# Kernel tuning notes

Hardware: AMD Instinct MI355X
Metric: run time of the kernel (lower is better)

The kernel has to match this reference:

```python
import jax, jax.numpy as jnp
import numpy as np

# ---- problem dims ----
B, S, C, H, W = 4, 8, 3, 256, 256
P = 68          # keypoints (self.points)
DS = 4          # detector downsample
WIN = 8
STEPS = 10      # Gauss-Newton iterations per frame pair
EPS = 1e-6
GRAY_W = jnp.array([0.299, 0.587, 0.114], dtype=jnp.float32)

# window offsets [K,2] in (x,y)
_rng = jnp.arange(-WIN, WIN + 1, dtype=jnp.float32)
_OFF = jnp.stack(jnp.meshgrid(_rng, _rng, indexing='xy'), -1).reshape(-1, 2)


def setup_inputs() -> dict:
    key = jax.random.key(0)
    k1, k2 = jax.random.split(key)
    inputs = jax.random.normal(k1, (B, S, C, H, W), dtype=jnp.float32)
    Wdet = jax.random.normal(k2, (P, C, 3, 3), dtype=jnp.float32) * 0.1
    bdet = jnp.zeros((P,), dtype=jnp.float32)
    return {"inputs": inputs, "Wdet": Wdet, "bdet": bdet}


def _bilinear(img, xy):
    # img [H,W]; xy [...,2] in (x,y) pixel coords -> sampled values [...]
    x = jnp.clip(xy[..., 0], 0.0, W - 1.001)
    y = jnp.clip(xy[..., 1], 0.0, H - 1.001)
    x0 = jnp.floor(x); y0 = jnp.floor(y)
    wx = x - x0; wy = y - y0
    x0i = x0.astype(jnp.int32); y0i = y0.astype(jnp.int32)
    x1i = jnp.minimum(x0i + 1, W - 1); y1i = jnp.minimum(y0i + 1, H - 1)
    v00 = img[y0i, x0i]; v01 = img[y0i, x1i]
    v10 = img[y1i, x0i]; v11 = img[y1i, x1i]
    return (1 - wy) * ((1 - wx) * v00 + wx * v01) + wy * ((1 - wx) * v10 + wx * v11)


def _grad_xy(img):
    # central differences with edge replication
    px = jnp.pad(img, ((0, 0), (1, 1)), mode='edge')
    py = jnp.pad(img, ((1, 1), (0, 0)), mode='edge')
    gx = (px[:, 2:] - px[:, :-2]) * 0.5
    gy = (py[2:, :] - py[:-2, :]) * 0.5
    return gx, gy


def _lk_track(old, new, pts):
    # one Lucas-Kanade tracking step: old/new [H,W] gray, pts [P,2] -> [P,2]
    gx, gy = _grad_xy(old)
    pos0 = pts[:, None, :] + _OFF[None]            # [P,K,2]
    I0 = _bilinear(old, pos0)                      # [P,K] template patch
    Ix = _bilinear(gx, pos0)
    Iy = _bilinear(gy, pos0)
    Gxx = (Ix * Ix).sum(-1); Gxy = (Ix * Iy).sum(-1); Gyy = (Iy * Iy).sum(-1)
    det = Gxx * Gyy - Gxy * Gxy + EPS
    Ginv = jnp.stack([jnp.stack([Gyy, -Gxy], -1),
                      jnp.stack([-Gxy, Gxx], -1)], -2) / det[:, None, None]  # [P,2,2]

    def step(i, v):
        I1 = _bilinear(new, pos0 + v[:, None, :])  # [P,K]
        err = I0 - I1
        b = jnp.stack([(err * Ix).sum(-1), (err * Iy).sum(-1)], -1)  # [P,2]
        return v + jnp.einsum('pij,pj->pi', Ginv, b)

    v = jax.lax.fori_loop(0, STEPS, step, jnp.zeros_like(pts))
    return pts + v


def _lk_forward_backward(gray, locs):
    # gray [S,H,W], locs [S,P,2] -> nextPts, fbackPts, backPts each [S,P,2]
    def f(pts, frames):
        o, n = frames
        q = _lk_track(o, n, pts)
        return q, q

    # forward: track detector locs of frame 0 through the sequence
    _, fout = jax.lax.scan(f, locs[0], (gray[:-1], gray[1:]))
    nextPts = jnp.concatenate([locs[:1], fout], 0)
    ro, rn = gray[1:][::-1], gray[:-1][::-1]
    # forward-backward: track the forward end point back to frame 0
    _, fbout = jax.lax.scan(f, nextPts[-1], (ro, rn))
    fbackPts = jnp.concatenate([nextPts[-1:], fbout], 0)[::-1]
    # backward: track detector locs of last frame back through the sequence
    _, bout = jax.lax.scan(f, locs[-1], (ro, rn))
    backPts = jnp.concatenate([locs[-1:], bout], 0)[::-1]
    return nextPts, fbackPts, backPts


def _detector(x, Wdet, bdet):
    # x [N,C,H,W] -> heatmaps [N,P,H/DS,W/DS], locs [N,P,2] (pixel coords), scores [N,P]
    hm = jax.lax.conv_general_dilated(
        x, Wdet, window_strides=(DS, DS), padding='SAME',
        dimension_numbers=('NCHW', 'OIHW', 'NCHW')) + bdet[None, :, None, None]
    N, _, Hd, Wd = hm.shape
    flat = hm.reshape(N, P, Hd * Wd)
    prob = jax.nn.softmax(flat, axis=-1)
    ys, xs = jnp.meshgrid(jnp.arange(Hd, dtype=hm.dtype),
                          jnp.arange(Wd, dtype=hm.dtype), indexing='ij')
    ex = (prob * xs.reshape(-1)).sum(-1) * DS   # soft-argmax, upscaled to input px
    ey = (prob * ys.reshape(-1)).sum(-1) * DS
    locs = jnp.stack([ex, ey], -1)
    scos = flat.max(-1)
    return hm, locs, scos


def reference(inputs, Wdet, bdet):
    x = inputs.reshape(B * S, C, H, W)
    hm, locs, scos = _detector(x, Wdet, bdet)
    heatmaps = hm.reshape(B, S, P, H // DS, W // DS)
    batch_locs = locs.reshape(B, S, P, 2)
    batch_scos = scos.reshape(B, S, P)
    gray = jnp.einsum('bschw,c->bshw', inputs, GRAY_W)  # [B,S,H,W]
    nextPts, fbackPts, backPts = jax.vmap(_lk_forward_backward)(gray, batch_locs)
    return heatmaps, batch_locs, batch_scos, nextPts, fbackPts, backPts
```

## Files before the change

kernel.cpp:

```cpp
#include <hip/hip_runtime.h>
#include <math.h>

namespace {
constexpr int Bn = 4, Sn = 8, Cn = 3, Himg = 256, Wimg = 256;
constexpr int Pn = 68, DS = 4, WIN = 8, STEPS = 10;
constexpr int HWi = Himg * Wimg;
constexpr int NIMG = Bn * Sn;
constexpr int HD = Himg / DS, WD = Wimg / DS;
constexpr int Kwin = (2 * WIN + 1) * (2 * WIN + 1);
constexpr int NWAVE = 5;
constexpr int TPB = NWAVE * 64;
}

__global__ __launch_bounds__(256) void gray_kernel(const float* __restrict__ in,
                                                   float* __restrict__ gray) {
    int idx = blockIdx.x * blockDim.x + threadIdx.x;
    int total = NIMG * HWi / 4;
    if (idx >= total) return;
    int img = idx / (HWi / 4);
    int off = idx % (HWi / 4);
    const float* base = in + (size_t)img * 3 * HWi;
    float4 c0 = ((const float4*)(base))[off];
    float4 c1 = ((const float4*)(base + HWi))[off];
    float4 c2 = ((const float4*)(base + 2 * HWi))[off];
    float4 g;
    g.x = 0.299f * c0.x + 0.587f * c1.x + 0.114f * c2.x;
    g.y = 0.299f * c0.y + 0.587f * c1.y + 0.114f * c2.y;
    g.z = 0.299f * c0.z + 0.587f * c1.z + 0.114f * c2.z;
    g.w = 0.299f * c0.w + 0.587f * c1.w + 0.114f * c2.w;
    ((float4*)(gray + (size_t)img * HWi))[off] = g;
}

__global__ __launch_bounds__(256) void conv_kernel(const float* __restrict__ x,
                                                   const float* __restrict__ Wdet,
                                                   const float* __restrict__ bdet,
                                                   float* __restrict__ hm) {
    __shared__ float wsh[Pn * 27];
    __shared__ float bsh[Pn];
    __shared__ float insh[3][3][Wimg];
    int n = blockIdx.x >> 6;
    int oy = blockIdx.x & 63;
    int tid = threadIdx.x;
    for (int t = tid; t < Pn * 27; t += 256) wsh[t] = Wdet[t];
    if (tid < Pn) bsh[tid] = bdet[tid];
    for (int t = tid; t < 3 * 3 * Wimg; t += 256) {
        int c = t / (3 * Wimg);
        int r = (t / Wimg) % 3;
        int col = t % Wimg;
        insh[c][r][col] = x[(size_t)n * 3 * HWi + (size_t)c * HWi + (oy * 4 + r) * Wimg + col];
    }
    __syncthreads();
    int ox = tid & 63;
    int wid = tid >> 6;
    float in_reg[27];
    #pragma unroll
    for (int c = 0; c < 3; c++)
        #pragma unroll
        for (int ky = 0; ky < 3; ky++)
            #pragma unroll
            for (int kx = 0; kx < 3; kx++)
                in_reg[c * 9 + ky * 3 + kx] = insh[c][ky][ox * 4 + kx];
    #pragma unroll
    for (int i = 0; i < 17; i++) {
        int p = wid + i * 4;
        const float* w = &wsh[p * 27];
        float acc = bsh[p];
        #pragma unroll
        for (int j = 0; j < 27; j++) acc += w[j] * in_reg[j];
        hm[(size_t)n * Pn * 4096 + (size_t)p * 4096 + oy * 64 + ox] = acc;
    }
}

__global__ __launch_bounds__(256) void smax_kernel(const float* __restrict__ hm,
                                                   float* __restrict__ locs,
                                                   float* __restrict__ scos) {
    int row = blockIdx.x;
    const float4* r = (const float4*)(hm + (size_t)row * 4096);
    int tid = threadIdx.x;
    float v[16];
    #pragma unroll
    for (int j = 0; j < 4; j++) {
        float4 q = r[tid + 256 * j];
        v[4 * j + 0] = q.x; v[4 * j + 1] = q.y; v[4 * j + 2] = q.z; v[4 * j + 3] = q.w;
    }
    float m = v[0];
    #pragma unroll
    for (int i = 1; i < 16; i++) m = fmaxf(m, v[i]);
    __shared__ float redm[4];
    #pragma unroll
    for (int o = 32; o; o >>= 1) m = fmaxf(m, __shfl_xor(m, o, 64));
    int wid = tid >> 6, lane = tid & 63;
    if (lane == 0) redm[wid] = m;
    __syncthreads();
    m = fmaxf(fmaxf(redm[0], redm[1]), fmaxf(redm[2], redm[3]));
    float s = 0.f, sx = 0.f, sy = 0.f;
    #pragma unroll
    for (int j = 0; j < 4; j++) {
        #pragma unroll
        for (int q = 0; q < 4; q++) {
            int e = (tid + 256 * j) * 4 + q;
            float ev = expf(v[4 * j + q] - m);
            s += ev;
            sx += ev * (float)(e & 63);
            sy += ev * (float)(e >> 6);
        }
    }
    #pragma unroll
    for (int o = 32; o; o >>= 1) {
        s  += __shfl_xor(s, o, 64);
        sx += __shfl_xor(sx, o, 64);
        sy += __shfl_xor(sy, o, 64);
    }
    __shared__ float reds[3][4];
    if (lane == 0) { reds[0][wid] = s; reds[1][wid] = sx; reds[2][wid] = sy; }
    __syncthreads();
    if (tid == 0) {
        float S_ = reds[0][0] + reds[0][1] + reds[0][2] + reds[0][3];
        float SX = reds[1][0] + reds[1][1] + reds[1][2] + reds[1][3];
        float SY = reds[2][0] + reds[2][1] + reds[2][2] + reds[2][3];
        locs[(size_t)row * 2 + 0] = SX / S_ * 4.0f;
        locs[(size_t)row * 2 + 1] = SY / S_ * 4.0f;
        scos[row] = m;
    }
}

template <int CTRL>
__device__ inline float dpp_add(float v) {
    int t = __builtin_amdgcn_update_dpp(0, __builtin_bit_cast(int, v), CTRL, 0xF, 0xF, true);
    return v + __builtin_bit_cast(float, t);
}

__device__ inline float wredw(float v) {
    v = dpp_add<0x111>(v);
    v = dpp_add<0x112>(v);
    v = dpp_add<0x114>(v);
    v = dpp_add<0x118>(v);
    v = dpp_add<0x142>(v);
    v = dpp_add<0x143>(v);
    int s = __builtin_amdgcn_readlane(__builtin_bit_cast(int, v), 63);
    return __builtin_bit_cast(float, s);
}

template <bool FLY>
__device__ inline float px_at(const float* __restrict__ im, int y, int x) {
    int i = y * Wimg + x;
    if constexpr (FLY)
        return 0.299f * im[i] + 0.587f * im[i + HWi] + 0.114f * im[i + 2 * HWi];
    else
        return im[i];
}

template <bool FLY>
__device__ inline float bilin(const float* __restrict__ im, float x, float y) {
    const float XM = (float)(Wimg - 1.001);
    const float YM = (float)(Himg - 1.001);
    x = fminf(fmaxf(x, 0.0f), XM);
    y = fminf(fmaxf(y, 0.0f), YM);
    float x0f = floorf(x), y0f = floorf(y);
    float wx = x - x0f, wy = y - y0f;
    int x0 = (int)x0f, y0 = (int)y0f;
    int x1 = min(x0 + 1, Wimg - 1), y1 = min(y0 + 1, Himg - 1);
    float v00 = px_at<FLY>(im, y0, x0);
    float v01 = px_at<FLY>(im, y0, x1);
    float v10 = px_at<FLY>(im, y1, x0);
    float v11 = px_at<FLY>(im, y1, x1);
    return (1.0f - wy) * ((1.0f - wx) * v00 + wx * v01) + wy * ((1.0f - wx) * v10 + wx * v11);
}

template <bool FLY>
__device__ inline void sample_tpl(const float* __restrict__ im, float x, float y,
                                  float& I0, float& Ix, float& Iy) {
    const float XM = (float)(Wimg - 1.001);
    const float YM = (float)(Himg - 1.001);
    x = fminf(fmaxf(x, 0.0f), XM);
    y = fminf(fmaxf(y, 0.0f), YM);
    float x0f = floorf(x), y0f = floorf(y);
    float wx = x - x0f, wy = y - y0f;
    int x0 = (int)x0f, y0 = (int)y0f;
    int x1 = min(x0 + 1, Wimg - 1), y1 = min(y0 + 1, Himg - 1);
    int xm = max(x0 - 1, 0), xp = min(x1 + 1, Wimg - 1);
    int ym = max(y0 - 1, 0), yp = min(y1 + 1, Himg - 1);
    float a_m0 = px_at<FLY>(im, ym, x0), a_m1 = px_at<FLY>(im, ym, x1);
    float a_0m = px_at<FLY>(im, y0, xm), a_00 = px_at<FLY>(im, y0, x0);
    float a_01 = px_at<FLY>(im, y0, x1), a_0p = px_at<FLY>(im, y0, xp);
    float a_1m = px_at<FLY>(im, y1, xm), a_10 = px_at<FLY>(im, y1, x0);
    float a_11 = px_at<FLY>(im, y1, x1), a_1p = px_at<FLY>(im, y1, xp);
    float a_p0 = px_at<FLY>(im, yp, x0), a_p1 = px_at<FLY>(im, yp, x1);
    float u = 1.0f - wx, t = 1.0f - wy;
    I0 = t * (u * a_00 + wx * a_01) + wy * (u * a_10 + wx * a_11);
    float gx00 = 0.5f * (a_01 - a_0m);
    float gx01 = 0.5f * (a_0p - a_00);
    float gx10 = 0.5f * (a_11 - a_1m);
    float gx11 = 0.5f * (a_1p - a_10);
    Ix = t * (u * gx00 + wx * gx01) + wy * (u * gx10 + wx * gx11);
    float gy00 = 0.5f * (a_10 - a_m0);
    float gy01 = 0.5f * (a_11 - a_m1);
    float gy10 = 0.5f * (a_p0 - a_00);
    float gy11 = 0.5f * (a_p1 - a_01);
    Iy = t * (u * gy00 + wx * gy01) + wy * (u * gy10 + wx * gy11);
}

template <bool FLY>
__device__ void lk_track(const float* __restrict__ oldI, const float* __restrict__ newI,
                         float& px, float& py, float dx, float dy, bool act,
                         int wid, int lane, float (*part)[NWAVE][3], int& evt) {
    float qx = px + dx, qy = py + dy;
    float I0 = 0.f, Ix = 0.f, Iy = 0.f;
    if (act) sample_tpl<FLY>(oldI, qx, qy, I0, Ix, Iy);
    float gxx = wredw(Ix * Ix);
    float gxy = wredw(Ix * Iy);
    float gyy = wredw(Iy * Iy);
    {
        int eb = evt & 1; evt++;
        if (lane == 0) { part[eb][wid][0] = gxx; part[eb][wid][1] = gxy; part[eb][wid][2] = gyy; }
        __syncthreads();
        gxx = 0.f; gxy = 0.f; gyy = 0.f;
        #pragma unroll
        for (int w = 0; w < NWAVE; w++) {
            gxx += part[eb][w][0]; gxy += part[eb][w][1]; gyy += part[eb][w][2];
        }
    }
    float det = gxx * gyy - gxy * gxy + 1e-6f;
    float A = gyy / det, Bv = -gxy / det, D = gxx / det;
    float vx = 0.f, vy = 0.f;
    for (int it = 0; it < STEPS; ++it) {
        float bx = 0.f, by = 0.f;
        if (act) {
            float I1 = bilin<FLY>(newI, qx + vx, qy + vy);
            float err = I0 - I1;
            bx = err * Ix;
            by = err * Iy;
        }
        bx = wredw(bx); by = wredw(by);
        int eb = evt & 1; evt++;
        if (lane == 0) { part[eb][wid][0] = bx; part[eb][wid][1] = by; }
        __syncthreads();
        bx = 0.f; by = 0.f;
        #pragma unroll
        for (int w = 0; w < NWAVE; w++) { bx += part[eb][w][0]; by += part[eb][w][1]; }
        vx += A * bx + Bv * by;
        vy += Bv * bx + D * by;
    }
    px += vx; py += vy;
}

template <bool FLY>
__global__ __launch_bounds__(TPB) void lk_kernel(const float* __restrict__ grayOrIn,
                                                 const float* __restrict__ locs,
                                                 float* __restrict__ nextPts,
                                                 float* __restrict__ fbackPts,
                                                 float* __restrict__ backPts) {
    constexpr size_t FS = FLY ? (size_t)3 * HWi : (size_t)HWi;
    __shared__ float part[2][NWAVE][3];
    int g = blockIdx.x;
    int typ = g / (Bn * Pn);
    int r = g % (Bn * Pn);
    int b = r / Pn;
    int p = r % Pn;
    int tid = threadIdx.x;
    int wid = tid >> 6, lane = tid & 63;
    bool act = tid < Kwin;
    int kk = act ? tid : 0;
    float dx = (float)(kk % 17 - 8);
    float dy = (float)(kk / 17 - 8);
    const float* G = grayOrIn + (size_t)b * Sn * FS;
    int evt = 0;
    auto LIDX = [&](int s) { return (((size_t)b * Sn + s) * Pn + p) * 2; };
    if (typ == 0) {
        float px = locs[LIDX(0)], py = locs[LIDX(0) + 1];
        if (tid == 0) { nextPts[LIDX(0)] = px; nextPts[LIDX(0) + 1] = py; }
        for (int s = 0; s < 7; s++) {
            lk_track<FLY>(G + s * FS, G + (s + 1) * FS, px, py, dx, dy, act, wid, lane, part, evt);
            if (tid == 0) { nextPts[LIDX(s + 1)] = px; nextPts[LIDX(s + 1) + 1] = py; }
        }
        if (tid == 0) { fbackPts[LIDX(7)] = px; fbackPts[LIDX(7) + 1] = py; }
        for (int i = 0; i < 7; i++) {
            lk_track<FLY>(G + (7 - i) * FS, G + (6 - i) * FS, px, py, dx, dy, act, wid, lane, part, evt);
            if (tid == 0) { fbackPts[LIDX(6 - i)] = px; fbackPts[LIDX(6 - i) + 1] = py; }
        }
    } else {
        float px = locs[LIDX(7)], py = locs[LIDX(7) + 1];
        if (tid == 0) { backPts[LIDX(7)] = px; backPts[LIDX(7) + 1] = py; }
        for (int i = 0; i < 7; i++) {
            lk_track<FLY>(G + (7 - i) * FS, G + (6 - i) * FS, px, py, dx, dy, act, wid, lane, part, evt);
            if (tid == 0) { backPts[LIDX(6 - i)] = px; backPts[LIDX(6 - i) + 1] = py; }
        }
    }
}

extern "C" void kernel_launch(void* const* d_in, const int* in_sizes, int n_in,
                              void* d_out, int out_size, void* d_ws, size_t ws_size,
                              hipStream_t stream) {
    const float* inputs = (const float*)d_in[0];
    const float* Wdet = (const float*)d_in[1];
    const float* bdet = (const float*)d_in[2];
    float* out = (float*)d_out;

    const size_t N_hm = (size_t)Bn * Sn * Pn * HD * WD;
    const size_t N_pts = (size_t)Bn * Sn * Pn * 2;
    float* hm = out;
    float* locs = out + N_hm;
    float* scos = locs + N_pts;
    float* nextPts = scos + (size_t)Bn * Sn * Pn;
    float* fbackPts = nextPts + N_pts;
    float* backPts = fbackPts + N_pts;

    conv_kernel<<<NIMG * 64, 256, 0, stream>>>(inputs, Wdet, bdet, hm);
    smax_kernel<<<NIMG * Pn, 256, 0, stream>>>(hm, locs, scos);

    const size_t gray_bytes = (size_t)NIMG * HWi * sizeof(float);
    if (ws_size >= gray_bytes) {
        float* gray = (float*)d_ws;
        gray_kernel<<<(NIMG * HWi / 4 + 255) / 256, 256, 0, stream>>>(inputs, gray);
        lk_kernel<false><<<2 * Bn * Pn, TPB, 0, stream>>>(gray, locs, nextPts, fbackPts, backPts);
    } else {
        lk_kernel<true><<<2 * Bn * Pn, TPB, 0, stream>>>(inputs, locs, nextPts, fbackPts, backPts);
    }
}
```

Before: 135.9 us.

## Track four keypoints per LK block with two samples per thread

The LK kernel now handles four keypoints per 256-thread block instead of one keypoint per 320-thread block. Each thread samples one or two window positions, and the per-wave partial sums for all four points share a single barrier per Gauss-Newton iteration. The aim is to cut the number of block-wide syncs per point and raise instruction-level parallelism in the latency-bound iteration loop. The cost is 136 blocks instead of 544, which may leave many compute units idle and lengthen the serial chain per block.

```diff
diff --git a/kernel.cpp b/kernel.cpp
--- a/kernel.cpp
+++ b/kernel.cpp
@@ -8,8 +8,8 @@
 constexpr int NIMG = Bn * Sn;
 constexpr int HD = Himg / DS, WD = Wimg / DS;
 constexpr int Kwin = (2 * WIN + 1) * (2 * WIN + 1);
-constexpr int NWAVE = 5;
-constexpr int TPB = NWAVE * 64;
+constexpr int CPB = 4;
+constexpr int TPB = 256;
 }
 
 __global__ __launch_bounds__(256) void gray_kernel(const float* __restrict__ in,
@@ -201,47 +201,80 @@
 }
 
 template <bool FLY>
-__device__ void lk_track(const float* __restrict__ oldI, const float* __restrict__ newI,
-                         float& px, float& py, float dx, float dy, bool act,
-                         int wid, int lane, float (*part)[NWAVE][3], int& evt) {
-    float qx = px + dx, qy = py + dy;
-    float I0 = 0.f, Ix = 0.f, Iy = 0.f;
-    if (act) sample_tpl<FLY>(oldI, qx, qy, I0, Ix, Iy);
-    float gxx = wredw(Ix * Ix);
-    float gxy = wredw(Ix * Iy);
-    float gyy = wredw(Iy * Iy);
-    {
+__device__ void lk_track4(const float* __restrict__ oldI, const float* __restrict__ newI,
+                          float* px, float* py,
+                          float dx0, float dy0, float dx1, float dy1, bool act1,
+                          int lane, int wid,
+                          float (*partG)[CPB][3][4], float (*partB)[CPB][2][4], int& evt) {
+    float I00[CPB], Ix0[CPB], Iy0[CPB];
+    float I01[CPB], Ix1[CPB], Iy1[CPB];
+    float A[CPB], Bv[CPB], D[CPB];
+    int ebG = evt & 1; evt++;
+    #pragma unroll
+    for (int c = 0; c < CPB; c++) {
+        float a = 0.f, b = 0.f, g = 0.f;
+        sample_tpl<FLY>(oldI, px[c] + dx0, py[c] + dy0, a, b, g);
+        I00[c] = a; Ix0[c] = b; Iy0[c] = g;
+        float a2 = 0.f, b2 = 0.f, g2 = 0.f;
+        if (act1) sample_tpl<FLY>(oldI, px[c] + dx1, py[c] + dy1, a2, b2, g2);
+        I01[c] = a2; Ix1[c] = b2; Iy1[c] = g2;
+        float gxx = wredw(b * b + b2 * b2);
+        float gxy = wredw(b * g + b2 * g2);
+        float gyy = wredw(g * g + g2 * g2);
+        if (lane == 0) {
+            partG[ebG][c][0][wid] = gxx;
+            partG[ebG][c][1][wid] = gxy;
+            partG[ebG][c][2][wid] = gyy;
+        }
+    }
+    __syncthreads();
+    #pragma unroll
+    for (int c = 0; c < CPB; c++) {
+        float4 g0 = *(const float4*)partG[ebG][c][0];
+        float4 g1 = *(const float4*)partG[ebG][c][1];
+        float4 g2 = *(const float4*)partG[ebG][c][2];
+        float gxx = g0.x + g0.y + g0.z + g0.w;
+        float gxy = g1.x + g1.y + g1.z + g1.w;
+        float gyy = g2.x + g2.y + g2.z + g2.w;
+        float det = gxx * gyy - gxy * gxy + 1e-6f;
+        A[c] = gyy / det; Bv[c] = -gxy / det; D[c] = gxx / det;
+    }
+    float vx[CPB], vy[CPB];
+    #pragma unroll
+    for (int c = 0; c < CPB; c++) { vx[c] = 0.f; vy[c] = 0.f; }
+    for (int it = 0; it < STEPS; ++it) {
         int eb = evt & 1; evt++;
-        if (lane == 0) { part[eb][wid][0] = gxx; part[eb][wid][1] = gxy; part[eb][wid][2] = gyy; }
+        #pragma unroll
+        for (int c = 0; c < CPB; c++) {
+            float I1 = bilin<FLY>(newI, px[c] + dx0 + vx[c], py[c] + dy0 + vy[c]);
+            float e0 = I00[c] - I1;
+            float bx = e0 * Ix0[c];
+            float by = e0 * Iy0[c];
+            if (act1) {
+                float I1b = bilin<FLY>(newI, px[c] + dx1 + vx[c], py[c] + dy1 + vy[c]);
+                float e1 = I01[c] - I1b;
+                bx += e1 * Ix1[c];
+                by += e1 * Iy1[c];
+            }
+            bx = wredw(bx); by = wredw(by);
+            if (lane == 0) {
+                partB[eb][c][0][wid] = bx;
+                partB[eb][c][1][wid] = by;
+            }
+        }
         __syncthreads();
-        gxx = 0.f; gxy = 0.f; gyy = 0.f;
-        #pragma unroll
-        for (int w = 0; w < NWAVE; w++) {
-            gxx += part[eb][w][0]; gxy += part[eb][w][1]; gyy += part[eb][w][2];
-        }
-    }
-    float det = gxx * gyy - gxy * gxy + 1e-6f;
-    float A = gyy / det, Bv = -gxy / det, D = gxx / det;
-    float vx = 0.f, vy = 0.f;
-    for (int it = 0; it < STEPS; ++it) {
-        float bx = 0.f, by = 0.f;
-        if (act) {
-            float I1 = bilin<FLY>(newI, qx + vx, qy + vy);
-            float err = I0 - I1;
-            bx = err * Ix;
-            by = err * Iy;
-        }
-        bx = wredw(bx); by = wredw(by);
-        int eb = evt & 1; evt++;
-        if (lane == 0) { part[eb][wid][0] = bx; part[eb][wid][1] = by; }
-        __syncthreads();
-        bx = 0.f; by = 0.f;
-        #pragma unroll
-        for (int w = 0; w < NWAVE; w++) { bx += part[eb][w][0]; by += part[eb][w][1]; }
-        vx += A * bx + Bv * by;
-        vy += Bv * bx + D * by;
-    }
-    px += vx; py += vy;
+        #pragma unroll
+        for (int c = 0; c < CPB; c++) {
+            float4 b0 = *(const float4*)partB[eb][c][0];
+            float4 b1 = *(const float4*)partB[eb][c][1];
+            float bx = b0.x + b0.y + b0.z + b0.w;
+            float by = b1.x + b1.y + b1.z + b1.w;
+            vx[c] += A[c] * bx + Bv[c] * by;
+            vy[c] += Bv[c] * bx + D[c] * by;
+        }
+    }
+    #pragma unroll
+    for (int c = 0; c < CPB; c++) { px[c] += vx[c]; py[c] += vy[c]; }
 }
 
 template <bool FLY>
@@ -251,39 +284,61 @@
                                                  float* __restrict__ fbackPts,
                                                  float* __restrict__ backPts) {
     constexpr size_t FS = FLY ? (size_t)3 * HWi : (size_t)HWi;
-    __shared__ float part[2][NWAVE][3];
+    constexpr int nb0 = (Bn * Pn) / CPB;
+    __shared__ float partG[2][CPB][3][4];
+    __shared__ float partB[2][CPB][2][4];
     int g = blockIdx.x;
-    int typ = g / (Bn * Pn);
-    int r = g % (Bn * Pn);
-    int b = r / Pn;
-    int p = r % Pn;
+    int typ = (g < nb0) ? 0 : 1;
+    int cb = (typ == 0 ? g : g - nb0) * CPB;
+    int b = cb / Pn;
+    int pb = cb % Pn;
     int tid = threadIdx.x;
-    int wid = tid >> 6, lane = tid & 63;
-    bool act = tid < Kwin;
-    int kk = act ? tid : 0;
-    float dx = (float)(kk % 17 - 8);
-    float dy = (float)(kk / 17 - 8);
+    int lane = tid & 63, wid = tid >> 6;
+    float dx0 = (float)(tid % 17 - 8);
+    float dy0 = (float)(tid / 17 - 8);
+    bool act1 = tid < (Kwin - 256);
+    int k1 = 256 + tid;
+    float dx1 = (float)(k1 % 17 - 8);
+    float dy1 = (float)(k1 / 17 - 8);
     const float* G = grayOrIn + (size_t)b * Sn * FS;
     int evt = 0;
-    auto LIDX = [&](int s) { return (((size_t)b * Sn + s) * Pn + p) * 2; };
+    auto LIDX = [&](int s, int c) { return (((size_t)b * Sn + s) * Pn + (pb + c)) * 2; };
+    float px[CPB], py[CPB];
     if (typ == 0) {
-        float px = locs[LIDX(0)], py = locs[LIDX(0) + 1];
-        if (tid == 0) { nextPts[LIDX(0)] = px; nextPts[LIDX(0) + 1] = py; }
+        #pragma unroll
+        for (int c = 0; c < CPB; c++) { px[c] = locs[LIDX(0, c)]; py[c] = locs[LIDX(0, c) + 1]; }
+        if (tid == 0)
+            #pragma unroll
+            for (int c = 0; c < CPB; c++) { nextPts[LIDX(0, c)] = px[c]; nextPts[LIDX(0, c) + 1] = py[c]; }
         for (int s = 0; s < 7; s++) {
-            lk_track<FLY>(G + s * FS, G + (s + 1) * FS, px, py, dx, dy, act, wid, lane, part, evt);
-            if (tid == 0) { nextPts[LIDX(s + 1)] = px; nextPts[LIDX(s + 1) + 1] = py; }
-        }
-        if (tid == 0) { fbackPts[LIDX(7)] = px; fbackPts[LIDX(7) + 1] = py; }
+            lk_track4<FLY>(G + s * FS, G + (s + 1) * FS, px, py, dx0, dy0, dx1, dy1, act1,
+                           lane, wid, partG, partB, evt);
+            if (tid == 0)
+                #pragma unroll
+                for (int c = 0; c < CPB; c++) { nextPts[LIDX(s + 1, c)] = px[c]; nextPts[LIDX(s + 1, c) + 1] = py[c]; }
+        }
+        if (tid == 0)
+            #pragma unroll
+            for (int c = 0; c < CPB; c++) { fbackPts[LIDX(7, c)] = px[c]; fbackPts[LIDX(7, c) + 1] = py[c]; }
         for (int i = 0; i < 7; i++) {
-            lk_track<FLY>(G + (7 - i) * FS, G + (6 - i) * FS, px, py, dx, dy, act, wid, lane, part, evt);
-            if (tid == 0) { fbackPts[LIDX(6 - i)] = px; fbackPts[LIDX(6 - i) + 1] = py; }
+            lk_track4<FLY>(G + (7 - i) * FS, G + (6 - i) * FS, px, py, dx0, dy0, dx1, dy1, act1,
+                           lane, wid, partG, partB, evt);
+            if (tid == 0)
+                #pragma unroll
+                for (int c = 0; c < CPB; c++) { fbackPts[LIDX(6 - i, c)] = px[c]; fbackPts[LIDX(6 - i, c) + 1] = py[c]; }
         }
     } else {
-        float px = locs[LIDX(7)], py = locs[LIDX(7) + 1];
-        if (tid == 0) { backPts[LIDX(7)] = px; backPts[LIDX(7) + 1] = py; }
+        #pragma unroll
+        for (int c = 0; c < CPB; c++) { px[c] = locs[LIDX(7, c)]; py[c] = locs[LIDX(7, c) + 1]; }
+        if (tid == 0)
+            #pragma unroll
+            for (int c = 0; c < CPB; c++) { backPts[LIDX(7, c)] = px[c]; backPts[LIDX(7, c) + 1] = py[c]; }
         for (int i = 0; i < 7; i++) {
-            lk_track<FLY>(G + (7 - i) * FS, G + (6 - i) * FS, px, py, dx, dy, act, wid, lane, part, evt);
-            if (tid == 0) { backPts[LIDX(6 - i)] = px; backPts[LIDX(6 - i) + 1] = py; }
+            lk_track4<FLY>(G + (7 - i) * FS, G + (6 - i) * FS, px, py, dx0, dy0, dx1, dy1, act1,
+                           lane, wid, partG, partB, evt);
+            if (tid == 0)
+                #pragma unroll
+                for (int c = 0; c < CPB; c++) { backPts[LIDX(6 - i, c)] = px[c]; backPts[LIDX(6 - i, c) + 1] = py[c]; }
         }
     }
 }
@@ -308,12 +363,13 @@
     conv_kernel<<<NIMG * 64, 256, 0, stream>>>(inputs, Wdet, bdet, hm);
     smax_kernel<<<NIMG * Pn, 256, 0, stream>>>(hm, locs, scos);
 
+    const int nblk = 2 * ((Bn * Pn) / CPB);
     const size_t gray_bytes = (size_t)NIMG * HWi * sizeof(float);
     if (ws_size >= gray_bytes) {
         float* gray = (float*)d_ws;
         gray_kernel<<<(NIMG * HWi / 4 + 255) / 256, 256, 0, stream>>>(inputs, gray);
-        lk_kernel<false><<<2 * Bn * Pn, TPB, 0, stream>>>(gray, locs, nextPts, fbackPts, backPts);
+        lk_kernel<false><<<nblk, TPB, 0, stream>>>(gray, locs, nextPts, fbackPts, backPts);
     } else {
-        lk_kernel<true><<<2 * Bn * Pn, TPB, 0, stream>>>(inputs, locs, nextPts, fbackPts, backPts);
-    }
-}
+        lk_kernel<true><<<nblk, TPB, 0, stream>>>(inputs, locs, nextPts, fbackPts, backPts);
+    }
+}
```

After: 326.8 us. +140.4%, slower.
